# Kernel optimization log

Measured on AMD Instinct MI355X. Metric: run time of the kernel, lower is better.

The kernel has to match this reference:

```python
import jax, jax.numpy as jnp
from jax import lax
import numpy as np

BETA = 0.25
K = 64   # num_embeddings
D = 64   # embedding_dim (must equal K per module's view(-1, D))
HID = 128
RES = 64
N_RES = 2


def _conv(x, w, b=None, stride=1, pad=0):
    y = lax.conv_general_dilated(x, w, (stride, stride), [(pad, pad), (pad, pad)],
                                 dimension_numbers=('NCHW', 'OIHW', 'NCHW'))
    if b is not None:
        y = y + b[None, :, None, None]
    return y


def _deconv(x, w, b, stride, pad):
    # torch ConvTranspose2d weight is (Cin, Cout, k, k); emulate via lhs-dilated conv with flipped kernel
    k = w.shape[2]
    p = k - 1 - pad
    w2 = jnp.transpose(w[:, :, ::-1, ::-1], (1, 0, 2, 3))  # -> (Cout, Cin, k, k)
    y = lax.conv_general_dilated(x, w2, (1, 1), [(p, p), (p, p)], lhs_dilation=(stride, stride),
                                 dimension_numbers=('NCHW', 'OIHW', 'NCHW'))
    return y + b[None, :, None, None]


def _res_block(x, w1, w2):
    # [Residual_Layer]*N_RES shares ONE set of weights; in-place ReLU means skip adds relu(x)
    for _ in range(N_RES):
        r = jax.nn.relu(x)
        h = _conv(r, w1, pad=1)
        h = jax.nn.relu(h)
        h = _conv(h, w2)
        x = r + h
    return jax.nn.relu(x)


def setup_inputs() -> dict:
    key = jax.random.key(0)
    ks = jax.random.split(key, 16)
    f32 = jnp.float32
    s = 0.05
    inp = {
        'x': jax.random.normal(ks[0], (32, 1, 256, 256), f32),
        # encoder
        'enc_c1_w': jax.random.normal(ks[1], (HID // 2, 1, 4, 4), f32) * s,
        'enc_c1_b': jnp.zeros((HID // 2,), f32),
        'enc_c2_w': jax.random.normal(ks[2], (HID, HID // 2, 4, 4), f32) * s,
        'enc_c2_b': jnp.zeros((HID,), f32),
        'enc_c3_w': jax.random.normal(ks[3], (HID, HID, 3, 3), f32) * s,
        'enc_c3_b': jnp.zeros((HID,), f32),
        'enc_r1_w': jax.random.normal(ks[4], (RES, HID, 3, 3), f32) * s,
        'enc_r2_w': jax.random.normal(ks[5], (HID, RES, 1, 1), f32) * s,
        # pre-VQ 1x1 conv: hidden -> K channels
        'vqc_w': jax.random.normal(ks[6], (K, HID, 1, 1), f32) * s,
        'vqc_b': jnp.zeros((K,), f32),
        # codebook, uniform(-1/K, 1/K)
        'emb': jax.random.uniform(ks[7], (K, D), f32, -1.0 / K, 1.0 / K),
        # decoder (ConvTranspose2d weights are (Cin, Cout, k, k))
        'dec_c1_w': jax.random.normal(ks[8], (D, HID, 3, 3), f32) * s,
        'dec_c1_b': jnp.zeros((HID,), f32),
        'dec_r1_w': jax.random.normal(ks[9], (RES, HID, 3, 3), f32) * s,
        'dec_r2_w': jax.random.normal(ks[10], (HID, RES, 1, 1), f32) * s,
        'dec_c2_w': jax.random.normal(ks[11], (HID, HID // 2, 4, 4), f32) * s,
        'dec_c2_b': jnp.zeros((HID // 2,), f32),
        'dec_c3_w': jax.random.normal(ks[12], (HID // 2, 1, 4, 4), f32) * s,
        'dec_c3_b': jnp.zeros((1,), f32),
    }
    return inp


def reference(x, enc_c1_w, enc_c1_b, enc_c2_w, enc_c2_b, enc_c3_w, enc_c3_b,
              enc_r1_w, enc_r2_w, vqc_w, vqc_b, emb,
              dec_c1_w, dec_c1_b, dec_r1_w, dec_r2_w, dec_c2_w, dec_c2_b, dec_c3_w, dec_c3_b):
    # ---- encoder ----
    h = jax.nn.relu(_conv(x, enc_c1_w, enc_c1_b, stride=2, pad=1))
    h = jax.nn.relu(_conv(h, enc_c2_w, enc_c2_b, stride=2, pad=1))
    h = _conv(h, enc_c3_w, enc_c3_b, pad=1)
    h = _res_block(h, enc_r1_w, enc_r2_w)
    z = _conv(h, vqc_w, vqc_b)  # (B, K, 64, 64)

    # ---- VQ ----
    zt = jnp.transpose(z, (0, 2, 3, 1))            # (B, H, W, D)
    flat = zt.reshape(-1, D)                        # (N, D)
    dist = (jnp.sum(flat ** 2, axis=1, keepdims=True)
            + jnp.sum(emb ** 2, axis=1)
            - 2.0 * flat @ emb.T)                   # (N, K)
    idx = jnp.argmin(dist, axis=1)                  # (N,)
    onehot = jax.nn.one_hot(idx, K, dtype=flat.dtype)
    q = (onehot @ emb).reshape(zt.shape)
    commitment = jnp.mean((lax.stop_gradient(q) - zt) ** 2)
    embedding_l = jnp.mean((q - lax.stop_gradient(zt)) ** 2)
    loss = commitment * BETA + embedding_l
    q_st = zt + lax.stop_gradient(q - zt)           # straight-through
    mean_enc = jnp.mean(onehot, axis=0)
    perplexity = jnp.exp(-jnp.sum(mean_enc * jnp.log(mean_enc + 1e-10)))
    qn = jnp.transpose(q_st, (0, 3, 1, 2))          # (B, D, 64, 64)

    # ---- decoder ----
    d = _deconv(qn, dec_c1_w, dec_c1_b, 1, 1)
    d = _res_block(d, dec_r1_w, dec_r2_w)
    d = jax.nn.relu(_deconv(d, dec_c2_w, dec_c2_b, 2, 1))
    x_re = jnp.tanh(_deconv(d, dec_c3_w, dec_c3_b, 2, 1))
    return (loss, x_re, perplexity, qn)
```

## Files before the change

kernel.cpp:

```cpp
#include <hip/hip_runtime.h>
#include <cmath>


static constexpr int NPOS  = 131072;
static constexpr long long NELEM = 8388608;

typedef __attribute__((ext_vector_type(8))) short short8;
typedef __attribute__((ext_vector_type(8))) unsigned short ushort8;
typedef __attribute__((ext_vector_type(4))) float f32x4;

__device__ __forceinline__ unsigned short f2bf(float f) {
  unsigned int x = __float_as_uint(f);
  unsigned int r = (x + 0x7fffu + ((x >> 16) & 1u)) >> 16;
  return (unsigned short)r;
}
__device__ __forceinline__ float bf2f(unsigned short u) {
  return __uint_as_float(((unsigned int)u) << 16);
}
__device__ __forceinline__ void split2(float v, unsigned short& h, unsigned short& l) {
  unsigned short hh = f2bf(v);
  h = hh;
  l = f2bf(v - bf2f(hh));
}

__global__ void __launch_bounds__(256) enc1_t(
    const float* __restrict__ in, const float* __restrict__ w,
    const float* __restrict__ bias,
    unsigned short* __restrict__ outh, unsigned short* __restrict__ outl)
{
  int tid = threadIdx.x;
  int rr = tid >> 7, ox = tid & 127;
  int oy  = blockIdx.x * 2 + rr;
  int oc0 = blockIdx.y * 16;
  int b   = blockIdx.z;

  const float* pl = in + (size_t)b * 65536;
  float v[16];
  #pragma unroll
  for (int ky = 0; ky < 4; ++ky) {
    int iy = 2 * oy - 1 + ky;
    #pragma unroll
    for (int kx = 0; kx < 4; ++kx) {
      int ix = 2 * ox - 1 + kx;
      v[ky * 4 + kx] = (iy >= 0 && iy < 256 && ix >= 0 && ix < 256)
                       ? pl[iy * 256 + ix] : 0.f;
    }
  }
  float acc[16];
  #pragma unroll
  for (int o = 0; o < 16; ++o) acc[o] = bias[oc0 + o];
  #pragma unroll
  for (int t = 0; t < 16; ++t)
    #pragma unroll
    for (int o = 0; o < 16; ++o)
      acc[o] += v[t] * w[(size_t)(oc0 + o) * 16 + t];

  size_t o = ((size_t)b * 16900 + (size_t)(oy + 1) * 130 + (ox + 1)) * 64 + oc0;
  ushort8 h0, h1, l0, l1;
  #pragma unroll
  for (int k = 0; k < 8; ++k) {
    unsigned short hh, ll;
    split2(fmaxf(acc[k], 0.f), hh, ll);      h0[k] = hh; l0[k] = ll;
    split2(fmaxf(acc[k + 8], 0.f), hh, ll);  h1[k] = hh; l1[k] = ll;
  }
  *(ushort8*)(outh + o)     = h0;
  *(ushort8*)(outh + o + 8) = h1;
  *(ushort8*)(outl + o)     = l0;
  *(ushort8*)(outl + o + 8) = l1;
}

template<int IC, int OC, bool BIAS, bool RELU>
__global__ void __launch_bounds__(256) mfma_enc3(
    const unsigned short* __restrict__ inh, const unsigned short* __restrict__ inl,
    const unsigned short* __restrict__ wh, const unsigned short* __restrict__ wl,
    const float* __restrict__ bias,
    unsigned short* __restrict__ outh, unsigned short* __restrict__ outl)
{
  constexpr int OM = OC / 16;
  constexpr int CP = 36;
  __shared__ unsigned short sh[6 * 66 * CP];
  __shared__ unsigned short sl[6 * 66 * CP];
  const int in_ss  = 4356 * IC;
  const int out_ss = 4356 * OC;
  const int tid = threadIdx.x;
  const int wv = tid >> 6, lane = tid & 63;
  const int quad = lane >> 4, l15 = lane & 15;

  const int id = blockIdx.x;
  const int xcd = id & 7;
  const int slot = id >> 3;
  const int bi = slot >> 4;
  const int yb = slot & 15;
  const int b = bi * 8 + xcd;
  const int y0 = yb * 4;
  const int y = y0 + wv;

  int xs[4];
  #pragma unroll
  for (int j = 0; j < 4; ++j) xs[j] = j * 16 + l15;
  const unsigned short* ibh = inh + (size_t)b * in_ss;
  const unsigned short* ibl = inl + (size_t)b * in_ss;

  f32x4 acc[OM][4];
  #pragma unroll
  for (int m = 0; m < OM; ++m) {
    const int oc0 = m * 16 + quad * 4;
    f32x4 ini = {0.f, 0.f, 0.f, 0.f};
    if (BIAS) {
      float4 bs = *(const float4*)(bias + oc0);
      ini[0] = bs.x; ini[1] = bs.y; ini[2] = bs.z; ini[3] = bs.w;
    }
    #pragma unroll
    for (int j = 0; j < 4; ++j) acc[m][j] = ini;
  }

  for (int k0 = 0; k0 < IC; k0 += 32) {
    for (int idx = tid; idx < 1584; idx += 256) {
      int row = idx / 264;
      int rem = idx - row * 264;
      int col = rem >> 2;
      int v = (rem & 3) << 3;
      size_t g = ((size_t)(y0 + row) * 66 + col) * IC + k0 + v;
      int s = (row * 66 + col) * CP + v;
      *(ushort8*)&sh[s] = *(const ushort8*)(ibh + g);
      *(ushort8*)&sl[s] = *(const ushort8*)(ibl + g);
    }
    __syncthreads();

    #pragma unroll
    for (int t = 0; t < 9; ++t) {
      const int dy = t / 3 - 1, dx = t % 3 - 1;
      short8 bh4[4], bl4[4];
      #pragma unroll
      for (int j = 0; j < 4; ++j) {
        int s = ((wv + dy + 1) * 66 + xs[j] + dx + 1) * CP + quad * 8;
        bh4[j] = *(const short8*)&sh[s];
        bl4[j] = *(const short8*)&sl[s];
      }
      const unsigned short* wrh = wh + (size_t)t * OC * IC + (size_t)l15 * IC + quad * 8 + k0;
      const unsigned short* wrl = wl + (size_t)t * OC * IC + (size_t)l15 * IC + quad * 8 + k0;
      #pragma unroll
      for (int m = 0; m < OM; ++m) {
        short8 ah = *(const short8*)(wrh + (size_t)m * 16 * IC);
        short8 al = *(const short8*)(wrl + (size_t)m * 16 * IC);
        #pragma unroll
        for (int j = 0; j < 4; ++j) {
          acc[m][j] = __builtin_amdgcn_mfma_f32_16x16x32_bf16(ah, bh4[j], acc[m][j], 0, 0, 0);
          acc[m][j] = __builtin_amdgcn_mfma_f32_16x16x32_bf16(ah, bl4[j], acc[m][j], 0, 0, 0);
          acc[m][j] = __builtin_amdgcn_mfma_f32_16x16x32_bf16(al, bh4[j], acc[m][j], 0, 0, 0);
        }
      }
    }
    __syncthreads();
  }

  #pragma unroll
  for (int m = 0; m < OM; ++m) {
    const int oc0 = m * 16 + quad * 4;
    #pragma unroll
    for (int j = 0; j < 4; ++j) {
      size_t o = (size_t)b * out_ss + ((size_t)(y + 1) * 66 + (xs[j] + 1)) * OC + oc0;
      ushort4 h4, l4;
      unsigned short hh, ll;
      float v;
      v = acc[m][j][0]; if (RELU) v = fmaxf(v, 0.f); split2(v, hh, ll); h4.x = hh; l4.x = ll;
      v = acc[m][j][1]; if (RELU) v = fmaxf(v, 0.f); split2(v, hh, ll); h4.y = hh; l4.y = ll;
      v = acc[m][j][2]; if (RELU) v = fmaxf(v, 0.f); split2(v, hh, ll); h4.z = hh; l4.z = ll;
      v = acc[m][j][3]; if (RELU) v = fmaxf(v, 0.f); split2(v, hh, ll); h4.w = hh; l4.w = ll;
      *(ushort4*)(outh + o) = h4;
      *(ushort4*)(outl + o) = l4;
    }
  }
}

template<int IC, int OC, bool HAS_BIAS, bool RELU>
__global__ void __launch_bounds__(256) mfma_dec3(
    const unsigned short* __restrict__ in, const unsigned short* __restrict__ wt,
    const float* __restrict__ bias, unsigned short* __restrict__ out)
{
  constexpr int OM = OC / 16;
  constexpr int CP = 36;
  __shared__ unsigned short sp[6 * 66 * CP];
  const int in_ss  = 4356 * IC;
  const int out_ss = 4356 * OC;
  const int tid = threadIdx.x;
  const int wv = tid >> 6, lane = tid & 63;
  const int quad = lane >> 4, l15 = lane & 15;

  const int id = blockIdx.x;
  const int xcd = id & 7;
  const int slot = id >> 3;
  const int bi = slot >> 4;
  const int yb = slot & 15;
  const int b = bi * 8 + xcd;
  const int y0 = yb * 4;
  const int y = y0 + wv;

  int xs[4];
  #pragma unroll
  for (int j = 0; j < 4; ++j) xs[j] = j * 16 + l15;
  const unsigned short* inb = in + (size_t)b * in_ss;

  f32x4 acc[OM][4];
  #pragma unroll
  for (int m = 0; m < OM; ++m) {
    const int oc0 = m * 16 + quad * 4;
    f32x4 ini = {0.f, 0.f, 0.f, 0.f};
    if (HAS_BIAS) {
      float4 bs = *(const float4*)(bias + oc0);
      ini[0] = bs.x; ini[1] = bs.y; ini[2] = bs.z; ini[3] = bs.w;
    }
    #pragma unroll
    for (int j = 0; j < 4; ++j) acc[m][j] = ini;
  }

  for (int k0 = 0; k0 < IC; k0 += 32) {
    for (int idx = tid; idx < 1584; idx += 256) {
      int row = idx / 264;
      int rem = idx - row * 264;
      int col = rem >> 2;
      int v = (rem & 3) << 3;
      size_t g = ((size_t)(y0 + row) * 66 + col) * IC + k0 + v;
      *(ushort8*)&sp[(row * 66 + col) * CP + v] = *(const ushort8*)(inb + g);
    }
    __syncthreads();

    #pragma unroll
    for (int t = 0; t < 9; ++t) {
      const int dy = t / 3 - 1, dx = t % 3 - 1;
      short8 fb[4];
      #pragma unroll
      for (int j = 0; j < 4; ++j) {
        int s = ((wv + dy + 1) * 66 + xs[j] + dx + 1) * CP + quad * 8;
        fb[j] = *(const short8*)&sp[s];
      }
      const unsigned short* wr = wt + (size_t)t * OC * IC + (size_t)l15 * IC + quad * 8 + k0;
      #pragma unroll
      for (int m = 0; m < OM; ++m) {
        short8 fa = *(const short8*)(wr + (size_t)m * 16 * IC);
        #pragma unroll
        for (int j = 0; j < 4; ++j)
          acc[m][j] = __builtin_amdgcn_mfma_f32_16x16x32_bf16(fa, fb[j], acc[m][j], 0, 0, 0);
      }
    }
    __syncthreads();
  }

  #pragma unroll
  for (int m = 0; m < OM; ++m) {
    const int oc0 = m * 16 + quad * 4;
    #pragma unroll
    for (int j = 0; j < 4; ++j) {
      unsigned short* o = out + (size_t)b * out_ss
                        + ((size_t)(y + 1) * 66 + (xs[j] + 1)) * OC + oc0;
      ushort4 u4;
      float v;
      v = acc[m][j][0]; if (RELU) v = fmaxf(v, 0.f); u4.x = f2bf(v);
      v = acc[m][j][1]; if (RELU) v = fmaxf(v, 0.f); u4.y = f2bf(v);
      v = acc[m][j][2]; if (RELU) v = fmaxf(v, 0.f); u4.z = f2bf(v);
      v = acc[m][j][3]; if (RELU) v = fmaxf(v, 0.f); u4.w = f2bf(v);
      *(ushort4*)o = u4;
    }
  }
}

template<int IC, int OC, int MODE, bool BIAS, bool RELU>
__global__ void __launch_bounds__(256) mfma_enc(
    const unsigned short* __restrict__ inh, const unsigned short* __restrict__ inl,
    const unsigned short* __restrict__ wh, const unsigned short* __restrict__ wl,
    const float* __restrict__ bias,
    const unsigned short* __restrict__ skh, const unsigned short* __restrict__ skl,
    unsigned short* __restrict__ outh, unsigned short* __restrict__ outl)
{
  constexpr int OM = OC / 16;
  constexpr int NT = (MODE == 0) ? 9 : ((MODE == 1) ? 16 : 1);
  constexpr int IW = (MODE == 1) ? 130 : 66;
  const int in_ss  = IW * IW * IC;
  const int out_ss = 4356 * OC;
  const int tid = threadIdx.x;
  const int wv = tid >> 6, lane = tid & 63;
  const int quad = lane >> 4, l15 = lane & 15;

  const int id = blockIdx.x;
  const int xcd = id & 7;
  const int slot = id >> 3;
  const int bi = slot >> 4;
  const int yb = slot & 15;
  const int b = bi * 8 + xcd;
  const int y = yb * 4 + wv;

  int xs[4];
  #pragma unroll
  for (int j = 0; j < 4; ++j) xs[j] = j * 16 + l15;
  const unsigned short* ibh = inh + (size_t)b * in_ss;
  const unsigned short* ibl = inl + (size_t)b * in_ss;

  f32x4 acc[OM][4];
  #pragma unroll
  for (int m = 0; m < OM; ++m) {
    const int oc0 = m * 16 + quad * 4;
    f32x4 ini = {0.f, 0.f, 0.f, 0.f};
    if (BIAS) {
      float4 bs = *(const float4*)(bias + oc0);
      ini[0] = bs.x; ini[1] = bs.y; ini[2] = bs.z; ini[3] = bs.w;
    }
    #pragma unroll
    for (int j = 0; j < 4; ++j) {
      f32x4 a = ini;
      if (MODE == 2) {
        size_t s = (size_t)b * out_ss + ((size_t)(y + 1) * 66 + (xs[j] + 1)) * OC + oc0;
        ushort4 sh = *(const ushort4*)(skh + s);
        ushort4 sl = *(const ushort4*)(skl + s);
        a[0] += bf2f(sh.x) + bf2f(sl.x);
        a[1] += bf2f(sh.y) + bf2f(sl.y);
        a[2] += bf2f(sh.z) + bf2f(sl.z);
        a[3] += bf2f(sh.w) + bf2f(sl.w);
      }
      acc[m][j] = a;
    }
  }

  for (int t = 0; t < NT; ++t) {
    int off[4];
    #pragma unroll
    for (int j = 0; j < 4; ++j) {
      if (MODE == 1)
        off[j] = ((2 * y + (t >> 2)) * 130 + (2 * xs[j] + (t & 3))) * IC;
      else
        off[j] = ((y + 1) * 66 + (xs[j] + 1)) * IC;
    }
    const unsigned short* wrh = wh + (size_t)t * OC * IC + (size_t)l15 * IC + quad * 8;
    const unsigned short* wrl = wl + (size_t)t * OC * IC + (size_t)l15 * IC + quad * 8;
    #pragma unroll
    for (int k0 = 0; k0 < IC; k0 += 32) {
      short8 bh[4], bl[4];
      #pragma unroll
      for (int j = 0; j < 4; ++j) {
        bh[j] = *(const short8*)(ibh + off[j] + quad * 8 + k0);
        bl[j] = *(const short8*)(ibl + off[j] + quad * 8 + k0);
      }
      #pragma unroll
      for (int m = 0; m < OM; ++m) {
        short8 ah = *(const short8*)(wrh + (size_t)m * 16 * IC + k0);
        short8 al = *(const short8*)(wrl + (size_t)m * 16 * IC + k0);
        #pragma unroll
        for (int j = 0; j < 4; ++j) {
          acc[m][j] = __builtin_amdgcn_mfma_f32_16x16x32_bf16(ah, bh[j], acc[m][j], 0, 0, 0);
          acc[m][j] = __builtin_amdgcn_mfma_f32_16x16x32_bf16(ah, bl[j], acc[m][j], 0, 0, 0);
          acc[m][j] = __builtin_amdgcn_mfma_f32_16x16x32_bf16(al, bh[j], acc[m][j], 0, 0, 0);
        }
      }
    }
  }

  #pragma unroll
  for (int m = 0; m < OM; ++m) {
    const int oc0 = m * 16 + quad * 4;
    #pragma unroll
    for (int j = 0; j < 4; ++j) {
      size_t o = (size_t)b * out_ss + ((size_t)(y + 1) * 66 + (xs[j] + 1)) * OC + oc0;
      ushort4 h4, l4;
      unsigned short hh, ll;
      float v;
      v = acc[m][j][0]; if (RELU) v = fmaxf(v, 0.f); split2(v, hh, ll); h4.x = hh; l4.x = ll;
      v = acc[m][j][1]; if (RELU) v = fmaxf(v, 0.f); split2(v, hh, ll); h4.y = hh; l4.y = ll;
      v = acc[m][j][2]; if (RELU) v = fmaxf(v, 0.f); split2(v, hh, ll); h4.z = hh; l4.z = ll;
      v = acc[m][j][3]; if (RELU) v = fmaxf(v, 0.f); split2(v, hh, ll); h4.w = hh; l4.w = ll;
      *(ushort4*)(outh + o) = h4;
      *(ushort4*)(outl + o) = l4;
    }
  }
}

__global__ void __launch_bounds__(256) vq_mfma(
    const unsigned short* __restrict__ xh, const unsigned short* __restrict__ xl,
    const unsigned short* __restrict__ wvh, const unsigned short* __restrict__ wvl,
    const unsigned short* __restrict__ evh, const unsigned short* __restrict__ evl,
    const float* __restrict__ emb, const float* __restrict__ e2,
    const float* __restrict__ vb,
    float* __restrict__ qn, unsigned short* __restrict__ dqb,
    float* __restrict__ sum_sq, int* __restrict__ hist)
{
  __shared__ float zsh[4][16][65];
  __shared__ int lh[64];
  const int tid = threadIdx.x;
  const int wv = tid >> 6, lane = tid & 63;
  const int quad = lane >> 4, l15 = lane & 15;
  const int y = blockIdx.x;
  const int b = blockIdx.z;
  const int x = wv * 16 + l15;
  if (tid < 64) lh[tid] = 0;

  f32x4 zacc[4];
  #pragma unroll
  for (int m = 0; m < 4; ++m) {
    float4 bv = *(const float4*)(vb + m * 16 + quad * 4);
    zacc[m][0] = bv.x; zacc[m][1] = bv.y; zacc[m][2] = bv.z; zacc[m][3] = bv.w;
  }
  size_t xoff = ((size_t)b * 4356 + (size_t)(y + 1) * 66 + (x + 1)) * 128;
  #pragma unroll
  for (int k0 = 0; k0 < 128; k0 += 32) {
    short8 bh = *(const short8*)(xh + xoff + k0 + quad * 8);
    short8 bl = *(const short8*)(xl + xoff + k0 + quad * 8);
    #pragma unroll
    for (int m = 0; m < 4; ++m) {
      short8 ah = *(const short8*)(wvh + (size_t)(m * 16 + l15) * 128 + k0 + quad * 8);
      short8 al = *(const short8*)(wvl + (size_t)(m * 16 + l15) * 128 + k0 + quad * 8);
      zacc[m] = __builtin_amdgcn_mfma_f32_16x16x32_bf16(ah, bh, zacc[m], 0, 0, 0);
      zacc[m] = __builtin_amdgcn_mfma_f32_16x16x32_bf16(ah, bl, zacc[m], 0, 0, 0);
      zacc[m] = __builtin_amdgcn_mfma_f32_16x16x32_bf16(al, bh, zacc[m], 0, 0, 0);
    }
  }

  float z2p = 0.f;
  #pragma unroll
  for (int m = 0; m < 4; ++m)
    #pragma unroll
    for (int r = 0; r < 4; ++r) {
      float zv = zacc[m][r];
      zsh[wv][l15][m * 16 + quad * 4 + r] = zv;
      z2p += zv * zv;
    }
  z2p += __shfl_xor(z2p, 16);
  z2p += __shfl_xor(z2p, 32);
  __syncthreads();

  f32x4 dacc[4];
  #pragma unroll
  for (int m = 0; m < 4; ++m) { dacc[m][0]=0.f; dacc[m][1]=0.f; dacc[m][2]=0.f; dacc[m][3]=0.f; }
  #pragma unroll
  for (int k0 = 0; k0 < 64; k0 += 32) {
    short8 bh, bl;
    #pragma unroll
    for (int j = 0; j < 8; ++j) {
      float zv = zsh[wv][l15][k0 + quad * 8 + j];
      unsigned short hh, ll;
      split2(zv, hh, ll);
      bh[j] = (short)hh; bl[j] = (short)ll;
    }
    #pragma unroll
    for (int m = 0; m < 4; ++m) {
      short8 ah = *(const short8*)(evh + (size_t)(m * 16 + l15) * 64 + k0 + quad * 8);
      short8 al = *(const short8*)(evl + (size_t)(m * 16 + l15) * 64 + k0 + quad * 8);
      dacc[m] = __builtin_amdgcn_mfma_f32_16x16x32_bf16(ah, bh, dacc[m], 0, 0, 0);
      dacc[m] = __builtin_amdgcn_mfma_f32_16x16x32_bf16(ah, bl, dacc[m], 0, 0, 0);
      dacc[m] = __builtin_amdgcn_mfma_f32_16x16x32_bf16(al, bh, dacc[m], 0, 0, 0);
    }
  }

  float best = INFINITY;
  int bidx = 64;
  #pragma unroll
  for (int m = 0; m < 4; ++m) {
    float4 e2v = *(const float4*)(e2 + m * 16 + quad * 4);
    #pragma unroll
    for (int r = 0; r < 4; ++r) {
      float e2s = (r == 0) ? e2v.x : (r == 1) ? e2v.y : (r == 2) ? e2v.z : e2v.w;
      float d = z2p + e2s - 2.f * dacc[m][r];
      int code = m * 16 + quad * 4 + r;
      if (d < best || (d == best && code < bidx)) { best = d; bidx = code; }
    }
  }
  {
    float ob = __shfl_xor(best, 16);
    int   oi = __shfl_xor(bidx, 16);
    if (ob < best || (ob == best && oi < bidx)) { best = ob; bidx = oi; }
    ob = __shfl_xor(best, 32);
    oi = __shfl_xor(bidx, 32);
    if (ob < best || (ob == best && oi < bidx)) { best = ob; bidx = oi; }
  }

  float ev[16];
  #pragma unroll
  for (int i = 0; i < 4; ++i) {
    float4 t = *(const float4*)(emb + (size_t)bidx * 64 + quad * 16 + i * 4);
    ev[i * 4] = t.x; ev[i * 4 + 1] = t.y; ev[i * 4 + 2] = t.z; ev[i * 4 + 3] = t.w;
  }
  float sq = 0.f;
  #pragma unroll
  for (int i = 0; i < 16; ++i) {
    float zv = zsh[wv][l15][quad * 16 + i];
    float df = ev[i] - zv;
    sq += df * df;
  }
  #pragma unroll
  for (int off = 1; off < 64; off <<= 1) sq += __shfl_xor(sq, off);
  if (lane == 0) atomicAdd(sum_sq, sq);
  if (quad == 0) atomicAdd(&lh[bidx], 1);

  int pos = y * 64 + x;
  float* qb = qn + (size_t)b * 262144 + (size_t)(quad * 16) * 4096 + pos;
  #pragma unroll
  for (int i = 0; i < 16; ++i) qb[(size_t)i * 4096] = ev[i];

  unsigned short* dq = dqb + ((size_t)b * 4356 + (size_t)(y + 1) * 66 + (x + 1)) * 64 + quad * 16;
  ushort8 d0, d1;
  #pragma unroll
  for (int i = 0; i < 8; ++i) { d0[i] = f2bf(ev[i]); d1[i] = f2bf(ev[i + 8]); }
  *(ushort8*)dq = d0;
  *(ushort8*)(dq + 8) = d1;

  __syncthreads();
  if (tid < 64) atomicAdd(&hist[tid], lh[tid]);
}

template<int IC, int OC, int MODE, bool HAS_BIAS, bool HAS_SKIP, bool RELU>
__global__ void __launch_bounds__(256) mfma_conv(
    const unsigned short* __restrict__ in, const unsigned short* __restrict__ wt,
    const float* __restrict__ bias, const unsigned short* __restrict__ skip,
    unsigned short* __restrict__ out, int in_ss, int out_ss)
{
  constexpr int OM = OC / 16;
  constexpr int NT = (MODE == 1) ? 4 : 1;
  constexpr int NP = (MODE == 1) ? 4 : 1;
  constexpr int PERB = 16 * NP;
  const int tid = threadIdx.x;
  const int wv = tid >> 6, lane = tid & 63;
  const int quad = lane >> 4, l15 = lane & 15;

  const int id = blockIdx.x;
  const int xcd = id & 7;
  const int slot = id >> 3;
  const int bi = slot / PERB;
  int r2 = slot - bi * PERB;
  int p = 0;
  if (MODE == 1) { p = r2 >> 4; r2 &= 15; }
  const int yb = r2;
  const int b = bi * 8 + xcd;
  const int y = yb * 4 + wv;

  int ry = 0, rx = 0;
  if (MODE == 1) {
    ry = p >> 1; rx = p & 1;
    wt  += (size_t)p * 4 * OC * IC;
    out += (size_t)p * 4356 * OC;
  }
  int xs[4];
  #pragma unroll
  for (int j = 0; j < 4; ++j) xs[j] = j * 16 + l15;
  const unsigned short* inb = in + (size_t)b * (size_t)in_ss;

  f32x4 acc[OM][4];
  #pragma unroll
  for (int m = 0; m < OM; ++m) {
    const int oc0 = m * 16 + quad * 4;
    f32x4 ini = {0.f, 0.f, 0.f, 0.f};
    if (HAS_BIAS) {
      float4 bs = *(const float4*)(bias + oc0);
      ini[0] = bs.x; ini[1] = bs.y; ini[2] = bs.z; ini[3] = bs.w;
    }
    #pragma unroll
    for (int j = 0; j < 4; ++j) {
      f32x4 a = ini;
      if (HAS_SKIP) {
        size_t s = (size_t)b * (size_t)out_ss + ((size_t)(y + 1) * 66 + (xs[j] + 1)) * OC + oc0;
        ushort4 sv = *(const ushort4*)(skip + s);
        a[0] += bf2f(sv.x); a[1] += bf2f(sv.y); a[2] += bf2f(sv.z); a[3] += bf2f(sv.w);
      }
      acc[m][j] = a;
    }
  }

  #pragma unroll
  for (int t = 0; t < NT; ++t) {
    const int dy = (MODE == 1) ? (ry - (t >> 1)) : 0;
    const int dx = (MODE == 1) ? (rx - (t & 1)) : 0;
    const unsigned short* wr = wt + (size_t)t * OC * IC + (size_t)l15 * IC + quad * 8;
    #pragma unroll
    for (int k0 = 0; k0 < IC; k0 += 32) {
      short8 fb[4];
      #pragma unroll
      for (int j = 0; j < 4; ++j)
        fb[j] = *(const short8*)(inb + ((size_t)(y + dy + 1) * 66 + (xs[j] + dx + 1)) * IC + quad * 8 + k0);
      #pragma unroll
      for (int m = 0; m < OM; ++m) {
        short8 fa = *(const short8*)(wr + (size_t)m * 16 * IC + k0);
        #pragma unroll
        for (int j = 0; j < 4; ++j)
          acc[m][j] = __builtin_amdgcn_mfma_f32_16x16x32_bf16(fa, fb[j], acc[m][j], 0, 0, 0);
      }
    }
  }

  #pragma unroll
  for (int m = 0; m < OM; ++m) {
    const int oc0 = m * 16 + quad * 4;
    #pragma unroll
    for (int j = 0; j < 4; ++j) {
      unsigned short* o = out + (size_t)b * (size_t)out_ss
                        + ((size_t)(y + 1) * 66 + (xs[j] + 1)) * OC + oc0;
      ushort4 u4;
      float v;
      v = acc[m][j][0]; if (RELU) v = fmaxf(v, 0.f); u4.x = f2bf(v);
      v = acc[m][j][1]; if (RELU) v = fmaxf(v, 0.f); u4.y = f2bf(v);
      v = acc[m][j][2]; if (RELU) v = fmaxf(v, 0.f); u4.z = f2bf(v);
      v = acc[m][j][3]; if (RELU) v = fmaxf(v, 0.f); u4.w = f2bf(v);
      *(ushort4*)o = u4;
    }
  }
}

__global__ void __launch_bounds__(256) dec3_t(
    const unsigned short* __restrict__ p4, const float* __restrict__ w,
    const float* __restrict__ bias, float* __restrict__ out)
{
  int tid = threadIdx.x;
  int yr = tid >> 7, x = tid & 127;
  int y  = blockIdx.x * 2 + yr;
  int b  = blockIdx.z;

  const int kt[2][2] = {{1, 3}, {0, 2}};
  const int dt[2][2] = {{1, 0}, {2, 1}};

  const unsigned short* base[9];
  #pragma unroll
  for (int dy = 0; dy < 3; ++dy) {
    int iy = y + dy - 1;
    int py = iy & 1, u = iy >> 1;
    #pragma unroll
    for (int dx = 0; dx < 3; ++dx) {
      int ix = x + dx - 1;
      int px = ix & 1, v = ix >> 1;
      base[dy * 3 + dx] = p4 + ((size_t)(b * 4 + py * 2 + px) * 4356
                                + (size_t)(u + 1) * 66 + (v + 1)) * 64;
    }
  }

  float acc[4] = {0.f, 0.f, 0.f, 0.f};
  for (int oct = 0; oct < 8; ++oct) {
    ushort8 s[9];
    #pragma unroll
    for (int t = 0; t < 9; ++t)
      s[t] = *(const ushort8*)(base[t] + oct * 8);

    #pragma unroll
    for (int j = 0; j < 8; ++j) {
      const float* wp = w + (size_t)(oct * 8 + j) * 16;
      float v9[9];
      #pragma unroll
      for (int t = 0; t < 9; ++t) v9[t] = bf2f(s[t][j]);
      #pragma unroll
      for (int ry = 0; ry < 2; ++ry)
        #pragma unroll
        for (int rx = 0; rx < 2; ++rx)
          #pragma unroll
          for (int a = 0; a < 2; ++a)
            #pragma unroll
            for (int c2 = 0; c2 < 2; ++c2)
              acc[ry * 2 + rx] += v9[dt[ry][a] * 3 + dt[rx][c2]]
                                * wp[kt[ry][a] * 4 + kt[rx][c2]];
    }
  }

  float b0 = bias[0];
  float* ob = out + (size_t)b * 65536;
  #pragma unroll
  for (int ry = 0; ry < 2; ++ry)
    #pragma unroll
    for (int rx = 0; rx < 2; ++rx)
      ob[(2 * y + ry) * 256 + 2 * x + rx] = tanhf(acc[ry * 2 + rx] + b0);
}

struct RingArgs {
  unsigned short* p[5];
  int icl[5];
  int H[5];
  int planes[5];
};
__global__ void rings_k(RingArgs a)
{
  int bi = blockIdx.y;
  if ((int)blockIdx.x >= a.planes[bi]) return;
  int H = a.H[bi];
  int icl = a.icl[bi];
  int C = 1 << icl;
  unsigned short* pl = a.p[bi] + (size_t)blockIdx.x * H * H * C;
  int cells = 4 * H - 4;
  int total = cells * C;
  for (int idx = threadIdx.x; idx < total; idx += 256) {
    int cell = idx >> icl;
    int e = idx & (C - 1);
    int row, col;
    if (cell < H)             { row = 0;     col = cell; }
    else if (cell < 2 * H)    { row = H - 1; col = cell - H; }
    else if (cell < 2 * H + (H - 2)) { row = cell - 2 * H + 1; col = 0; }
    else                      { row = cell - 2 * H - (H - 2) + 1; col = H - 1; }
    pl[((size_t)row * H + col) * C + e] = 0;
  }
}

__global__ void repack_k(const float* __restrict__ c1w, const float* __restrict__ r1w,
                         const float* __restrict__ r2w, const float* __restrict__ c2w,
                         unsigned short* __restrict__ W)
{
  int idx = blockIdx.x * 256 + threadIdx.x;
  if (idx >= 286720) return;
  float val;
  if (idx < 73728) {
    int t = idx / 8192, rem = idx & 8191;
    int oc = rem >> 6, ic = rem & 63;
    int ky = t / 3, kx = t - ky * 3;
    val = c1w[((ic * 128 + oc) * 3 + (2 - ky)) * 3 + (2 - kx)];
  } else if (idx < 147456) {
    int j = idx - 73728;
    int t = j / 8192, rem = j & 8191;
    int oc = rem >> 7, ic = rem & 127;
    int ky = t / 3, kx = t - ky * 3;
    val = r1w[((oc * 128 + ic) * 3 + ky) * 3 + kx];
  } else if (idx < 155648) {
    int j = idx - 147456;
    int oc = j >> 6, ic = j & 63;
    val = r2w[oc * 64 + ic];
  } else {
    int j = idx - 155648;
    int p = j >> 15;
    int t2 = (j >> 13) & 3;
    int oc = (j >> 7) & 63;
    int ic = j & 127;
    int ry = p >> 1, rx = p & 1;
    int aY = t2 >> 1, aX = t2 & 1;
    int ky = aY ? (3 - ry) : (1 - ry);
    int kx = aX ? (3 - rx) : (1 - rx);
    val = c2w[((ic * 64 + oc) * 4 + ky) * 4 + kx];
  }
  W[idx] = f2bf(val);
}

__global__ void repack_enc_k(const float* __restrict__ c2w, const float* __restrict__ c3w,
                             const float* __restrict__ r1w, const float* __restrict__ r2w,
                             unsigned short* __restrict__ Wh, unsigned short* __restrict__ Wl)
{
  int idx = blockIdx.x * 256 + threadIdx.x;
  if (idx >= 360448) return;
  float val;
  if (idx < 131072) {
    int t = idx >> 13;
    int rem = idx & 8191;
    int oc = rem >> 6, ic = rem & 63;
    val = c2w[(((size_t)oc * 64 + ic) << 4) + t];
  } else if (idx < 278528) {
    int j = idx - 131072;
    int t = j / 16384;
    int rem = j & 16383;
    int oc = rem >> 7, ic = rem & 127;
    val = c3w[((size_t)oc * 128 + ic) * 9 + t];
  } else if (idx < 352256) {
    int j = idx - 278528;
    int t = j / 8192;
    int rem = j & 8191;
    int oc = rem >> 7, ic = rem & 127;
    val = r1w[((size_t)oc * 128 + ic) * 9 + t];
  } else {
    int j = idx - 352256;
    int oc = j >> 6, ic = j & 63;
    val = r2w[oc * 64 + ic];
  }
  unsigned short h = f2bf(val);
  Wh[idx] = h;
  Wl[idx] = f2bf(val - bf2f(h));
}

__global__ void repack_vq_k(const float* __restrict__ vqw, const float* __restrict__ emb,
                            unsigned short* __restrict__ wvh, unsigned short* __restrict__ wvl,
                            unsigned short* __restrict__ evh, unsigned short* __restrict__ evl,
                            float* __restrict__ e2)
{
  int idx = blockIdx.x * 256 + threadIdx.x;
  if (idx < 8192) {
    float v = vqw[idx];
    unsigned short h = f2bf(v);
    wvh[idx] = h;
    wvl[idx] = f2bf(v - bf2f(h));
  } else if (idx < 12288) {
    int j = idx - 8192;
    float v = emb[j];
    unsigned short h = f2bf(v);
    evh[j] = h;
    evl[j] = f2bf(v - bf2f(h));
  }
  if (idx < 64) {
    float s = 0.f;
    for (int d = 0; d < 64; ++d) { float e = emb[idx * 64 + d]; s += e * e; }
    e2[idx] = s;
  }
}

__global__ void init_k(float* sum_sq, int* hist)
{
  int t = threadIdx.x;
  if (t == 0) sum_sq[0] = 0.f;
  if (t < 64) hist[t] = 0;
}

__global__ void finalize_k(const float* __restrict__ sum_sq, const int* __restrict__ hist,
                           float* __restrict__ loss_out, float* __restrict__ perp_out)
{
  if (threadIdx.x == 0) {
    float mse = sum_sq[0] / (float)NELEM;
    loss_out[0] = 1.25f * mse;
    float ent = 0.f;
    for (int k = 0; k < 64; ++k) {
      float p = (float)hist[k] / (float)NPOS;
      ent += p * logf(p + 1e-10f);
    }
    perp_out[0] = expf(-ent);
  }
}

extern "C" void kernel_launch(void* const* d_in, const int* in_sizes, int n_in,
                              void* d_out, int out_size, void* d_ws, size_t ws_size,
                              hipStream_t stream)
{
  const float* x        = (const float*)d_in[0];
  const float* enc_c1_w = (const float*)d_in[1];
  const float* enc_c1_b = (const float*)d_in[2];
  const float* enc_c2_w = (const float*)d_in[3];
  const float* enc_c2_b = (const float*)d_in[4];
  const float* enc_c3_w = (const float*)d_in[5];
  const float* enc_c3_b = (const float*)d_in[6];
  const float* enc_r1_w = (const float*)d_in[7];
  const float* enc_r2_w = (const float*)d_in[8];
  const float* vqc_w    = (const float*)d_in[9];
  const float* vqc_b    = (const float*)d_in[10];
  const float* emb      = (const float*)d_in[11];
  const float* dec_c1_w = (const float*)d_in[12];
  const float* dec_c1_b = (const float*)d_in[13];
  const float* dec_r1_w = (const float*)d_in[14];
  const float* dec_r2_w = (const float*)d_in[15];
  const float* dec_c2_w = (const float*)d_in[16];
  const float* dec_c2_b = (const float*)d_in[17];
  const float* dec_c3_w = (const float*)d_in[18];
  const float* dec_c3_b = (const float*)d_in[19];

  float* out      = (float*)d_out;
  float* loss_out = out;
  float* xre_out  = out + 1;
  float* perp_out = out + 1 + 2097152;
  float* qn_out   = out + 2 + 2097152;

  float* sum_sq = (float*)d_ws;
  int*   hist   = (int*)d_ws + 1;
  char*  pool   = (char*)d_ws + 1024;

  unsigned short* Wd  = (unsigned short*)(pool + 0);
  unsigned short* Weh = (unsigned short*)(pool + 600000);
  unsigned short* Wel = (unsigned short*)(pool + 1400000);
  unsigned short* Wvh = (unsigned short*)(pool + 2121728);
  unsigned short* Wvl = (unsigned short*)(pool + 2138112);
  unsigned short* Evh = (unsigned short*)(pool + 2154496);
  unsigned short* Evl = (unsigned short*)(pool + 2162688);
  float*          E2  = (float*)(pool + 2170880);
  unsigned short* E1h = (unsigned short*)(pool + 2200000);
  unsigned short* E1l = (unsigned short*)(pool + 71500000);
  unsigned short* B2h = (unsigned short*)(pool + 141000000);
  unsigned short* B2l = (unsigned short*)(pool + 177000000);
  unsigned short* R0h = (unsigned short*)(pool + 2200000);
  unsigned short* R0l = (unsigned short*)(pool + 38000000);
  unsigned short* Hh  = (unsigned short*)(pool + 74000000);
  unsigned short* Hl  = (unsigned short*)(pool + 92000000);
  unsigned short* X1h = (unsigned short*)(pool + 141000000);
  unsigned short* X1l = (unsigned short*)(pool + 177000000);
  unsigned short* X2h = (unsigned short*)(pool + 2200000);
  unsigned short* X2l = (unsigned short*)(pool + 38000000);
  unsigned short* Dq  = (unsigned short*)(pool + 213000000);
  unsigned short* Y1  = (unsigned short*)(pool + 141000000);
  unsigned short* S   = (unsigned short*)(pool + 110000000);
  unsigned short* Y2  = (unsigned short*)(pool + 177000000);
  unsigned short* P4  = (unsigned short*)(pool + 2200000);

  const int SS64  = 278784;
  const int SS128 = 557568;
  const int SSP4  = 1115136;

  hipLaunchKernelGGL(init_k, dim3(1), dim3(128), 0, stream, sum_sq, hist);
  hipLaunchKernelGGL(repack_k, dim3(1120), dim3(256), 0, stream,
                     dec_c1_w, dec_r1_w, dec_r2_w, dec_c2_w, Wd);
  hipLaunchKernelGGL(repack_enc_k, dim3(1408), dim3(256), 0, stream,
                     enc_c2_w, enc_c3_w, enc_r1_w, enc_r2_w, Weh, Wel);
  hipLaunchKernelGGL(repack_vq_k, dim3(48), dim3(256), 0, stream,
                     vqc_w, emb, Wvh, Wvl, Evh, Evl, E2);

  {
    RingArgs a;
    a.p[0] = E1h; a.icl[0] = 6; a.H[0] = 130; a.planes[0] = 32;
    a.p[1] = E1l; a.icl[1] = 6; a.H[1] = 130; a.planes[1] = 32;
    a.p[2] = B2h; a.icl[2] = 7; a.H[2] = 66;  a.planes[2] = 32;
    a.p[3] = B2l; a.icl[3] = 7; a.H[3] = 66;  a.planes[3] = 32;
    a.p[4] = Dq;  a.icl[4] = 6; a.H[4] = 66;  a.planes[4] = 32;
    hipLaunchKernelGGL(rings_k, dim3(32, 5), dim3(256), 0, stream, a);
  }

  hipLaunchKernelGGL(enc1_t, dim3(64, 4, 32), dim3(256), 0, stream,
                     x, enc_c1_w, enc_c1_b, E1h, E1l);
  hipLaunchKernelGGL((mfma_enc<64, 128, 1, true, true>),
                     dim3(512), dim3(256), 0, stream,
                     E1h, E1l, Weh, Wel, enc_c2_b, nullptr, nullptr, B2h, B2l);

  {
    RingArgs a;
    a.p[0] = R0h; a.icl[0] = 7; a.H[0] = 66; a.planes[0] = 32;
    a.p[1] = R0l; a.icl[1] = 7; a.H[1] = 66; a.planes[1] = 32;
    a.p[2] = Hh;  a.icl[2] = 6; a.H[2] = 66; a.planes[2] = 32;
    a.p[3] = Hl;  a.icl[3] = 6; a.H[3] = 66; a.planes[3] = 32;
    a.p[4] = S;   a.icl[4] = 6; a.H[4] = 66; a.planes[4] = 32;
    hipLaunchKernelGGL(rings_k, dim3(32, 5), dim3(256), 0, stream, a);
  }

  hipLaunchKernelGGL((mfma_enc3<128, 128, true, true>),
                     dim3(512), dim3(256), 0, stream,
                     B2h, B2l, Weh + 131072, Wel + 131072, enc_c3_b, R0h, R0l);

  {
    RingArgs a;
    a.p[0] = X1h; a.icl[0] = 7; a.H[0] = 66; a.planes[0] = 32;
    a.p[1] = X1l; a.icl[1] = 7; a.H[1] = 66; a.planes[1] = 32;
    a.p[2] = nullptr; a.icl[2] = 0; a.H[2] = 2; a.planes[2] = 0;
    a.p[3] = nullptr; a.icl[3] = 0; a.H[3] = 2; a.planes[3] = 0;
    a.p[4] = nullptr; a.icl[4] = 0; a.H[4] = 2; a.planes[4] = 0;
    hipLaunchKernelGGL(rings_k, dim3(32, 2), dim3(256), 0, stream, a);
  }

  hipLaunchKernelGGL((mfma_enc3<128, 64, false, true>),
                     dim3(512), dim3(256), 0, stream,
                     R0h, R0l, Weh + 278528, Wel + 278528, nullptr, Hh, Hl);
  hipLaunchKernelGGL((mfma_enc<64, 128, 2, false, true>),
                     dim3(512), dim3(256), 0, stream,
                     Hh, Hl, Weh + 352256, Wel + 352256, nullptr,
                     R0h, R0l, X1h, X1l);

  {
    RingArgs a;
    a.p[0] = X2h; a.icl[0] = 7; a.H[0] = 66; a.planes[0] = 32;
    a.p[1] = X2l; a.icl[1] = 7; a.H[1] = 66; a.planes[1] = 32;
    a.p[2] = nullptr; a.icl[2] = 0; a.H[2] = 2; a.planes[2] = 0;
    a.p[3] = nullptr; a.icl[3] = 0; a.H[3] = 2; a.planes[3] = 0;
    a.p[4] = nullptr; a.icl[4] = 0; a.H[4] = 2; a.planes[4] = 0;
    hipLaunchKernelGGL(rings_k, dim3(32, 2), dim3(256), 0, stream, a);
  }

  hipLaunchKernelGGL((mfma_enc3<128, 64, false, true>),
                     dim3(512), dim3(256), 0, stream,
                     X1h, X1l, Weh + 278528, Wel + 278528, nullptr, Hh, Hl);
  hipLaunchKernelGGL((mfma_enc<64, 128, 2, false, true>),
                     dim3(512), dim3(256), 0, stream,
                     Hh, Hl, Weh + 352256, Wel + 352256, nullptr,
                     X1h, X1l, X2h, X2l);

  hipLaunchKernelGGL(vq_mfma, dim3(64, 1, 32), dim3(256), 0, stream,
                     X2h, X2l, Wvh, Wvl, Evh, Evl, emb, E2, vqc_b,
                     qn_out, Dq, sum_sq, hist);

  {
    RingArgs a;
    a.p[0] = Y1;  a.icl[0] = 7; a.H[0] = 66; a.planes[0] = 32;
    a.p[1] = Y2;  a.icl[1] = 7; a.H[1] = 66; a.planes[1] = 32;
    a.p[2] = P4;  a.icl[2] = 6; a.H[2] = 66; a.planes[2] = 128;
    a.p[3] = nullptr; a.icl[3] = 0; a.H[3] = 2; a.planes[3] = 0;
    a.p[4] = nullptr; a.icl[4] = 0; a.H[4] = 2; a.planes[4] = 0;
    hipLaunchKernelGGL(rings_k, dim3(128, 3), dim3(256), 0, stream, a);
  }

  hipLaunchKernelGGL((mfma_dec3<64, 128, true, true>),
                     dim3(512), dim3(256), 0, stream,
                     Dq, Wd, dec_c1_b, Y1);
  hipLaunchKernelGGL((mfma_dec3<128, 64, false, true>),
                     dim3(512), dim3(256), 0, stream,
                     Y1, Wd + 73728, nullptr, S);
  hipLaunchKernelGGL((mfma_conv<64, 128, 2, false, true, true>),
                     dim3(512), dim3(256), 0, stream,
                     S, Wd + 147456, nullptr, Y1, Y2, SS64, SS128);
  hipLaunchKernelGGL((mfma_dec3<128, 64, false, true>),
                     dim3(512), dim3(256), 0, stream,
                     Y2, Wd + 73728, nullptr, S);
  hipLaunchKernelGGL((mfma_conv<64, 128, 2, false, true, true>),
                     dim3(512), dim3(256), 0, stream,
                     S, Wd + 147456, nullptr, Y2, Y1, SS64, SS128);

  hipLaunchKernelGGL((mfma_conv<128, 64, 1, true, false, true>),
                     dim3(2048), dim3(256), 0, stream,
                     Y1, Wd + 155648, dec_c2_b, nullptr, P4, SS128, SSP4);

  hipLaunchKernelGGL(dec3_t, dim3(64, 1, 32), dim3(256), 0, stream,
                     P4, dec_c3_w, dec_c3_b, xre_out);

  hipLaunchKernelGGL(finalize_k, dim3(1), dim3(64), 0, stream,
                     sum_sq, hist, loss_out, perp_out);
}
```

Measured before the change: 1.696 ms.

## Store enc1 output in 4 parity-split planes and stage enc2 inputs in LDS

The first encoder conv now writes its output into four polyphase (even/odd row × column) padded 66x66 planes instead of one 130x130 padded image. A new enc2 kernel loads each phase tile into shared memory and runs the stride-2 4x4 conv as four stride-1 2x2 sub-convolutions with MFMA, which replaces strided global gathers with contiguous LDS reads. The generic mfma_enc template is reduced to a 1x1 residual-only kernel. In exchange the workspace layout changes, ring padding must cover 128 planes, and the new kernel adds extra __syncthreads barriers.

```diff
diff --git a/kernel.cpp b/kernel.cpp
--- a/kernel.cpp
+++ b/kernel.cpp
@@ -55,7 +55,10 @@
     for (int o = 0; o < 16; ++o)
       acc[o] += v[t] * w[(size_t)(oc0 + o) * 16 + t];
 
-  size_t o = ((size_t)b * 16900 + (size_t)(oy + 1) * 130 + (ox + 1)) * 64 + oc0;
+  int pp = ((oy & 1) << 1) | (ox & 1);
+  int u = oy >> 1, vv = ox >> 1;
+  size_t o = ((size_t)(b * 4 + pp)) * 278784
+           + ((size_t)(u + 1) * 66 + (vv + 1)) * 64 + oc0;
   ushort8 h0, h1, l0, l1;
   #pragma unroll
   for (int k = 0; k < 8; ++k) {
@@ -67,6 +70,116 @@
   *(ushort8*)(outh + o + 8) = h1;
   *(ushort8*)(outl + o)     = l0;
   *(ushort8*)(outl + o + 8) = l1;
+}
+
+__global__ void __launch_bounds__(256) mfma_enc2p(
+    const unsigned short* __restrict__ inh, const unsigned short* __restrict__ inl,
+    const unsigned short* __restrict__ wh, const unsigned short* __restrict__ wl,
+    const float* __restrict__ bias,
+    unsigned short* __restrict__ outh, unsigned short* __restrict__ outl)
+{
+  constexpr int IC = 64, OC = 128, OM = 8, CP = 36;
+  __shared__ unsigned short sh[6 * 66 * CP];
+  __shared__ unsigned short sl[6 * 66 * CP];
+  const int out_ss = 4356 * OC;
+  const int tid = threadIdx.x;
+  const int wv = tid >> 6, lane = tid & 63;
+  const int quad = lane >> 4, l15 = lane & 15;
+
+  const int id = blockIdx.x;
+  const int xcd = id & 7;
+  const int slot = id >> 3;
+  const int bi = slot >> 4;
+  const int yb = slot & 15;
+  const int b = bi * 8 + xcd;
+  const int y0 = yb * 4;
+  const int y = y0 + wv;
+
+  int xs[4];
+  #pragma unroll
+  for (int j = 0; j < 4; ++j) xs[j] = j * 16 + l15;
+
+  f32x4 acc[OM][4];
+  #pragma unroll
+  for (int m = 0; m < OM; ++m) {
+    const int oc0 = m * 16 + quad * 4;
+    float4 bs = *(const float4*)(bias + oc0);
+    f32x4 ini;
+    ini[0] = bs.x; ini[1] = bs.y; ini[2] = bs.z; ini[3] = bs.w;
+    #pragma unroll
+    for (int j = 0; j < 4; ++j) acc[m][j] = ini;
+  }
+
+  for (int k0 = 0; k0 < IC; k0 += 32) {
+    #pragma unroll
+    for (int pp = 0; pp < 4; ++pp) {
+      const int py = pp >> 1, px = pp & 1;
+      const unsigned short* pbh = inh + (size_t)(b * 4 + pp) * 278784;
+      const unsigned short* pbl = inl + (size_t)(b * 4 + pp) * 278784;
+      for (int idx = tid; idx < 1584; idx += 256) {
+        int row = idx / 264;
+        int rem = idx - row * 264;
+        int col = rem >> 2;
+        int v = (rem & 3) << 3;
+        size_t g = ((size_t)(y0 + row) * 66 + col) * IC + k0 + v;
+        int s = (row * 66 + col) * CP + v;
+        *(ushort8*)&sh[s] = *(const ushort8*)(pbh + g);
+        *(ushort8*)&sl[s] = *(const ushort8*)(pbl + g);
+      }
+      __syncthreads();
+
+      #pragma unroll
+      for (int a = 0; a < 2; ++a) {
+        const int ky = py ? (2 * a) : (1 + 2 * a);
+        const int du = py ? (a - 1) : a;
+        #pragma unroll
+        for (int c2 = 0; c2 < 2; ++c2) {
+          const int kx = px ? (2 * c2) : (1 + 2 * c2);
+          const int dv = px ? (c2 - 1) : c2;
+          const int t = ky * 4 + kx;
+          short8 bh4[4], bl4[4];
+          #pragma unroll
+          for (int j = 0; j < 4; ++j) {
+            int s = ((wv + du + 1) * 66 + xs[j] + dv + 1) * CP + quad * 8;
+            bh4[j] = *(const short8*)&sh[s];
+            bl4[j] = *(const short8*)&sl[s];
+          }
+          const unsigned short* wrh = wh + (size_t)t * OC * IC + (size_t)l15 * IC + quad * 8 + k0;
+          const unsigned short* wrl = wl + (size_t)t * OC * IC + (size_t)l15 * IC + quad * 8 + k0;
+          #pragma unroll
+          for (int m = 0; m < OM; ++m) {
+            short8 ah = *(const short8*)(wrh + (size_t)m * 16 * IC);
+            short8 al = *(const short8*)(wrl + (size_t)m * 16 * IC);
+            #pragma unroll
+            for (int j = 0; j < 4; ++j) {
+              acc[m][j] = __builtin_amdgcn_mfma_f32_16x16x32_bf16(ah, bh4[j], acc[m][j], 0, 0, 0);
+              acc[m][j] = __builtin_amdgcn_mfma_f32_16x16x32_bf16(ah, bl4[j], acc[m][j], 0, 0, 0);
+              acc[m][j] = __builtin_amdgcn_mfma_f32_16x16x32_bf16(al, bh4[j], acc[m][j], 0, 0, 0);
+            }
+          }
+        }
+      }
+      __syncthreads();
+    }
+  }
+
+  #pragma unroll
+  for (int m = 0; m < OM; ++m) {
+    const int oc0 = m * 16 + quad * 4;
+    #pragma unroll
+    for (int j = 0; j < 4; ++j) {
+      size_t o = (size_t)b * out_ss + ((size_t)(y + 1) * 66 + (xs[j] + 1)) * OC + oc0;
+      ushort4 h4, l4;
+      unsigned short hh, ll;
+      float v;
+      v = fmaxf(acc[m][j][0], 0.f); split2(v, hh, ll); h4.x = hh; l4.x = ll;
+      v = fmaxf(acc[m][j][1], 0.f); split2(v, hh, ll); h4.y = hh; l4.y = ll;
+      v = fmaxf(acc[m][j][2], 0.f); split2(v, hh, ll); h4.z = hh; l4.z = ll;
+      v = fmaxf(acc[m][j][3], 0.f); split2(v, hh, ll); h4.w = hh; l4.w = ll;
+      *(ushort4*)(outh + o) = h4;
+      *(ushort4*)(outl + o) = l4;
+    }
+  }
 }
 
 template<int IC, int OC, bool BIAS, bool RELU>
@@ -264,18 +377,15 @@
   }
 }
 
-template<int IC, int OC, int MODE, bool BIAS, bool RELU>
-__global__ void __launch_bounds__(256) mfma_enc(
+template<int IC, int OC, bool RELU>
+__global__ void __launch_bounds__(256) mfma_enc1x1(
     const unsigned short* __restrict__ inh, const unsigned short* __restrict__ inl,
     const unsigned short* __restrict__ wh, const unsigned short* __restrict__ wl,
-    const float* __restrict__ bias,
     const unsigned short* __restrict__ skh, const unsigned short* __restrict__ skl,
     unsigned short* __restrict__ outh, unsigned short* __restrict__ outl)
 {
   constexpr int OM = OC / 16;
-  constexpr int NT = (MODE == 0) ? 9 : ((MODE == 1) ? 16 : 1);
-  constexpr int IW = (MODE == 1) ? 130 : 66;
-  const int in_ss  = IW * IW * IC;
+  const int in_ss  = 4356 * IC;
   const int out_ss = 4356 * OC;
   const int tid = threadIdx.x;
   const int wv = tid >> 6, lane = tid & 63;
@@ -299,56 +409,40 @@
   #pragma unroll
   for (int m = 0; m < OM; ++m) {
     const int oc0 = m * 16 + quad * 4;
-    f32x4 ini = {0.f, 0.f, 0.f, 0.f};
-    if (BIAS) {
-      float4 bs = *(const float4*)(bias + oc0);
-      ini[0] = bs.x; ini[1] = bs.y; ini[2] = bs.z; ini[3] = bs.w;
-    }
     #pragma unroll
     for (int j = 0; j < 4; ++j) {
-      f32x4 a = ini;
-      if (MODE == 2) {
-        size_t s = (size_t)b * out_ss + ((size_t)(y + 1) * 66 + (xs[j] + 1)) * OC + oc0;
-        ushort4 sh = *(const ushort4*)(skh + s);
-        ushort4 sl = *(const ushort4*)(skl + s);
-        a[0] += bf2f(sh.x) + bf2f(sl.x);
-        a[1] += bf2f(sh.y) + bf2f(sl.y);
-        a[2] += bf2f(sh.z) + bf2f(sl.z);
-        a[3] += bf2f(sh.w) + bf2f(sl.w);
-      }
+      f32x4 a;
+      size_t s = (size_t)b * out_ss + ((size_t)(y + 1) * 66 + (xs[j] + 1)) * OC + oc0;
+      ushort4 sh = *(const ushort4*)(skh + s);
+      ushort4 sl = *(const ushort4*)(skl + s);
+      a[0] = bf2f(sh.x) + bf2f(sl.x);
+      a[1] = bf2f(sh.y) + bf2f(sl.y);
+      a[2] = bf2f(sh.z) + bf2f(sl.z);
+      a[3] = bf2f(sh.w) + bf2f(sl.w);
       acc[m][j] = a;
     }
   }
 
-  for (int t = 0; t < NT; ++t) {
-    int off[4];
+  const unsigned short* wrh = wh + (size_t)l15 * IC + quad * 8;
+  const unsigned short* wrl = wl + (size_t)l15 * IC + quad * 8;
+  #pragma unroll
+  for (int k0 = 0; k0 < IC; k0 += 32) {
+    short8 bh[4], bl[4];
     #pragma unroll
     for (int j = 0; j < 4; ++j) {
-      if (MODE == 1)
-        off[j] = ((2 * y + (t >> 2)) * 130 + (2 * xs[j] + (t & 3))) * IC;
-      else
-        off[j] = ((y + 1) * 66 + (xs[j] + 1)) * IC;
-    }
-    const unsigned short* wrh = wh + (size_t)t * OC * IC + (size_t)l15 * IC + quad * 8;
-    const unsigned short* wrl = wl + (size_t)t * OC * IC + (size_t)l15 * IC + quad * 8;
-    #pragma unroll
-    for (int k0 = 0; k0 < IC; k0 += 32) {
-      short8 bh[4], bl[4];
+      int off = ((y + 1) * 66 + (xs[j] + 1)) * IC;
+      bh[j] = *(const short8*)(ibh + off + quad * 8 + k0);
+      bl[j] = *(const short8*)(ibl + off + quad * 8 + k0);
+    }
+    #pragma unroll
+    for (int m = 0; m < OM; ++m) {
+      short8 ah = *(const short8*)(wrh + (size_t)m * 16 * IC + k0);
+      short8 al = *(const short8*)(wrl + (size_t)m * 16 * IC + k0);
       #pragma unroll
       for (int j = 0; j < 4; ++j) {
-        bh[j] = *(const short8*)(ibh + off[j] + quad * 8 + k0);
-        bl[j] = *(const short8*)(ibl + off[j] + quad * 8 + k0);
-      }
-      #pragma unroll
-      for (int m = 0; m < OM; ++m) {
-        short8 ah = *(const short8*)(wrh + (size_t)m * 16 * IC + k0);
-        short8 al = *(const short8*)(wrl + (size_t)m * 16 * IC + k0);
-        #pragma unroll
-        for (int j = 0; j < 4; ++j) {
-          acc[m][j] = __builtin_amdgcn_mfma_f32_16x16x32_bf16(ah, bh[j], acc[m][j], 0, 0, 0);
-          acc[m][j] = __builtin_amdgcn_mfma_f32_16x16x32_bf16(ah, bl[j], acc[m][j], 0, 0, 0);
-          acc[m][j] = __builtin_amdgcn_mfma_f32_16x16x32_bf16(al, bh[j], acc[m][j], 0, 0, 0);
-        }
+        acc[m][j] = __builtin_amdgcn_mfma_f32_16x16x32_bf16(ah, bh[j], acc[m][j], 0, 0, 0);
+        acc[m][j] = __builtin_amdgcn_mfma_f32_16x16x32_bf16(ah, bl[j], acc[m][j], 0, 0, 0);
+        acc[m][j] = __builtin_amdgcn_mfma_f32_16x16x32_bf16(al, bh[j], acc[m][j], 0, 0, 0);
       }
     }
   }
@@ -842,31 +936,31 @@
   int*   hist   = (int*)d_ws + 1;
   char*  pool   = (char*)d_ws + 1024;
 
-  unsigned short* Wd  = (unsigned short*)(pool + 0);
-  unsigned short* Weh = (unsigned short*)(pool + 600000);
-  unsigned short* Wel = (unsigned short*)(pool + 1400000);
-  unsigned short* Wvh = (unsigned short*)(pool + 2121728);
-  unsigned short* Wvl = (unsigned short*)(pool + 2138112);
-  unsigned short* Evh = (unsigned short*)(pool + 2154496);
-  unsigned short* Evl = (unsigned short*)(pool + 2162688);
-  float*          E2  = (float*)(pool + 2170880);
-  unsigned short* E1h = (unsigned short*)(pool + 2200000);
-  unsigned short* E1l = (unsigned short*)(pool + 71500000);
-  unsigned short* B2h = (unsigned short*)(pool + 141000000);
-  unsigned short* B2l = (unsigned short*)(pool + 177000000);
-  unsigned short* R0h = (unsigned short*)(pool + 2200000);
-  unsigned short* R0l = (unsigned short*)(pool + 38000000);
-  unsigned short* Hh  = (unsigned short*)(pool + 74000000);
-  unsigned short* Hl  = (unsigned short*)(pool + 92000000);
-  unsigned short* X1h = (unsigned short*)(pool + 141000000);
-  unsigned short* X1l = (unsigned short*)(pool + 177000000);
-  unsigned short* X2h = (unsigned short*)(pool + 2200000);
-  unsigned short* X2l = (unsigned short*)(pool + 38000000);
-  unsigned short* Dq  = (unsigned short*)(pool + 213000000);
-  unsigned short* Y1  = (unsigned short*)(pool + 141000000);
-  unsigned short* S   = (unsigned short*)(pool + 110000000);
-  unsigned short* Y2  = (unsigned short*)(pool + 177000000);
-  unsigned short* P4  = (unsigned short*)(pool + 2200000);
+  unsigned short* Wd   = (unsigned short*)(pool + 0);
+  unsigned short* Weh  = (unsigned short*)(pool + 600000);
+  unsigned short* Wel  = (unsigned short*)(pool + 1400000);
+  unsigned short* Wvh  = (unsigned short*)(pool + 2121728);
+  unsigned short* Wvl  = (unsigned short*)(pool + 2138112);
+  unsigned short* Evh  = (unsigned short*)(pool + 2154496);
+  unsigned short* Evl  = (unsigned short*)(pool + 2162688);
+  float*          E2   = (float*)(pool + 2170880);
+  unsigned short* E1ph = (unsigned short*)(pool + 2200000);
+  unsigned short* E1pl = (unsigned short*)(pool + 73600000);
+  unsigned short* B2h  = (unsigned short*)(pool + 145000000);
+  unsigned short* B2l  = (unsigned short*)(pool + 181000000);
+  unsigned short* R0h  = (unsigned short*)(pool + 2200000);
+  unsigned short* R0l  = (unsigned short*)(pool + 38000000);
+  unsigned short* Hh   = (unsigned short*)(pool + 74000000);
+  unsigned short* Hl   = (unsigned short*)(pool + 92000000);
+  unsigned short* S    = (unsigned short*)(pool + 110000000);
+  unsigned short* X1h  = (unsigned short*)(pool + 145000000);
+  unsigned short* X1l  = (unsigned short*)(pool + 181000000);
+  unsigned short* X2h  = (unsigned short*)(pool + 2200000);
+  unsigned short* X2l  = (unsigned short*)(pool + 38000000);
+  unsigned short* Dq   = (unsigned short*)(pool + 217000000);
+  unsigned short* Y1   = (unsigned short*)(pool + 145000000);
+  unsigned short* Y2   = (unsigned short*)(pool + 181000000);
+  unsigned short* P4   = (unsigned short*)(pool + 2200000);
 
   const int SS64  = 278784;
   const int SS128 = 557568;
@@ -882,19 +976,18 @@
 
   {
     RingArgs a;
-    a.p[0] = E1h; a.icl[0] = 6; a.H[0] = 130; a.planes[0] = 32;
-    a.p[1] = E1l; a.icl[1] = 6; a.H[1] = 130; a.planes[1] = 32;
-    a.p[2] = B2h; a.icl[2] = 7; a.H[2] = 66;  a.planes[2] = 32;
-    a.p[3] = B2l; a.icl[3] = 7; a.H[3] = 66;  a.planes[3] = 32;
-    a.p[4] = Dq;  a.icl[4] = 6; a.H[4] = 66;  a.planes[4] = 32;
-    hipLaunchKernelGGL(rings_k, dim3(32, 5), dim3(256), 0, stream, a);
+    a.p[0] = E1ph; a.icl[0] = 6; a.H[0] = 66; a.planes[0] = 128;
+    a.p[1] = E1pl; a.icl[1] = 6; a.H[1] = 66; a.planes[1] = 128;
+    a.p[2] = B2h;  a.icl[2] = 7; a.H[2] = 66; a.planes[2] = 32;
+    a.p[3] = B2l;  a.icl[3] = 7; a.H[3] = 66; a.planes[3] = 32;
+    a.p[4] = Dq;   a.icl[4] = 6; a.H[4] = 66; a.planes[4] = 32;
+    hipLaunchKernelGGL(rings_k, dim3(128, 5), dim3(256), 0, stream, a);
   }
 
   hipLaunchKernelGGL(enc1_t, dim3(64, 4, 32), dim3(256), 0, stream,
-                     x, enc_c1_w, enc_c1_b, E1h, E1l);
-  hipLaunchKernelGGL((mfma_enc<64, 128, 1, true, true>),
-                     dim3(512), dim3(256), 0, stream,
-                     E1h, E1l, Weh, Wel, enc_c2_b, nullptr, nullptr, B2h, B2l);
+                     x, enc_c1_w, enc_c1_b, E1ph, E1pl);
+  hipLaunchKernelGGL(mfma_enc2p, dim3(512), dim3(256), 0, stream,
+                     E1ph, E1pl, Weh, Wel, enc_c2_b, B2h, B2l);
 
   {
     RingArgs a;
@@ -923,10 +1016,9 @@
   hipLaunchKernelGGL((mfma_enc3<128, 64, false, true>),
                      dim3(512), dim3(256), 0, stream,
                      R0h, R0l, Weh + 278528, Wel + 278528, nullptr, Hh, Hl);
-  hipLaunchKernelGGL((mfma_enc<64, 128, 2, false, true>),
+  hipLaunchKernelGGL((mfma_enc1x1<64, 128, true>),
                      dim3(512), dim3(256), 0, stream,
-                     Hh, Hl, Weh + 352256, Wel + 352256, nullptr,
-                     R0h, R0l, X1h, X1l);
+                     Hh, Hl, Weh + 352256, Wel + 352256, R0h, R0l, X1h, X1l);
 
   {
     RingArgs a;
@@ -941,10 +1033,9 @@
   hipLaunchKernelGGL((mfma_enc3<128, 64, false, true>),
                      dim3(512), dim3(256), 0, stream,
                      X1h, X1l, Weh + 278528, Wel + 278528, nullptr, Hh, Hl);
-  hipLaunchKernelGGL((mfma_enc<64, 128, 2, false, true>),
+  hipLaunchKernelGGL((mfma_enc1x1<64, 128, true>),
                      dim3(512), dim3(256), 0, stream,
-                     Hh, Hl, Weh + 352256, Wel + 352256, nullptr,
-                     X1h, X1l, X2h, X2l);
+                     Hh, Hl, Weh + 352256, Wel + 352256, X1h, X1l, X2h, X2l);
 
   hipLaunchKernelGGL(vq_mfma, dim3(64, 1, 32), dim3(256), 0, stream,
                      X2h, X2l, Wvh, Wvl, Evh, Evl, emb, E2, vqc_b,
```

New measurement: 1.863 ms. 9.8% more time.
